# Kernel tuning notes

Hardware: AMD Instinct MI355X
Metric: run time of the kernel (lower is better)

## Reference

```python
import jax, jax.numpy as jnp
import numpy as np

N = 20000      # nodes (all graphs in batch)
E = 320000     # edges (avg degree 16)
G = 16         # graphs in batch
D_IN = 32      # raw node feature dim
D_LAP = 16     # laplacian PE dim
D = 256        # d_model
H = 8          # heads
DH = D // H    # head dim
L = 2          # encoder layers
D_FF = 2 * D   # FFN hidden (FFN_layer1: d_model -> 2*d_model)
EPS = 1e-5


def _layer_norm(x, g, b):
    m = jnp.mean(x, axis=-1, keepdims=True)
    v = jnp.var(x, axis=-1, keepdims=True)
    return g * (x - m) * jax.lax.rsqrt(v + EPS) + b


def setup_inputs() -> dict:
    key = jax.random.key(0)
    ks = jax.random.split(key, 32)

    feat = jax.random.normal(ks[0], (N, D_IN), dtype=jnp.float32)
    lap_pos = jax.random.normal(ks[1], (N, D_LAP), dtype=jnp.float32)
    # random +-1 sign flip per PE dim (done with torch.rand in the original forward)
    sign_flip = jnp.where(jax.random.uniform(ks[2], (D_LAP,)) >= 0.5, 1.0, -1.0).astype(jnp.float32)

    src = jax.random.randint(ks[3], (E,), 0, N, dtype=jnp.int32)
    dst = jax.random.randint(ks[4], (E,), 0, N, dtype=jnp.int32)
    graph_ids = jnp.sort(jax.random.randint(ks[5], (N,), 0, G, dtype=jnp.int32))

    def xavier(k, shape):
        fan_in, fan_out = shape[-2], shape[-1]
        lim = np.sqrt(6.0 / (fan_in + fan_out))
        return jax.random.uniform(k, shape, minval=-lim, maxval=lim, dtype=jnp.float32)

    inp = {
        "feat": feat, "lap_pos": lap_pos, "sign_flip": sign_flip,
        "src": src, "dst": dst, "graph_ids": graph_ids,
        # input embeddings
        "Wh": xavier(ks[6], (D_IN, D)), "bh": jnp.zeros((D,), jnp.float32),
        "Wlp": xavier(ks[7], (D_LAP, D)), "blp": jnp.zeros((D,), jnp.float32),
        # per-layer params, stacked on leading layer axis
        "Wq": xavier(ks[8], (L, D, D)), "Wk": xavier(ks[9], (L, D, D)),
        "Wv": xavier(ks[10], (L, D, D)),
        "Wo": xavier(ks[11], (L, D, D)), "bo": jnp.zeros((L, D), jnp.float32),
        "g1": jnp.ones((L, D), jnp.float32), "b1": jnp.zeros((L, D), jnp.float32),
        "W1": xavier(ks[12], (L, D, D_FF)), "c1": jnp.zeros((L, D_FF), jnp.float32),
        "W2": xavier(ks[13], (L, D_FF, D)), "c2": jnp.zeros((L, D), jnp.float32),
        "g2": jnp.ones((L, D), jnp.float32), "b2": jnp.zeros((L, D), jnp.float32),
    }
    return inp


def _forward(feat, lap_pos, sign_flip, src, dst, graph_ids,
             Wh, bh, Wlp, blp, Wq, Wk, Wv, Wo, bo, g1, b1, W1, c1, W2, c2, g2, b2):
    scale = np.sqrt(DH).astype(np.float32)

    h = feat @ Wh + bh                                  # [N, D]
    h = h + (lap_pos * sign_flip[None, :]) @ Wlp + blp  # add PE embedding

    for l in range(L):
        h_in1 = h
        Q = (h @ Wq[l]).reshape(N, H, DH)
        K = (h @ Wk[l]).reshape(N, H, DH)
        V = (h @ Wv[l]).reshape(N, H, DH)

        # per-edge dot-product score, then exp(clamp(score/sqrt(dh), -5, 5))
        score = jnp.sum(K[src] * Q[dst], axis=-1)                       # [E, H]
        s = jnp.exp(jnp.clip(score / scale, -5.0, 5.0))                # [E, H]

        # segment softmax of s over incoming edges per dst node (F.softmax on mailbox)
        m = jax.ops.segment_max(s, dst, num_segments=N)                 # [N, H], -inf if no in-edges
        p = jnp.exp(s - m[dst])                                         # [E, H]
        den = jax.ops.segment_sum(p, dst, num_segments=N)               # [N, H]
        msg = jax.ops.segment_sum(p[:, :, None] * V[src], dst, num_segments=N)  # [N, H, DH]
        attn = msg / jnp.where(den > 0, den, 1.0)[:, :, None]
        attn = attn.reshape(N, D)

        h = _layer_norm(h_in1 + attn @ Wo[l] + bo[l], g1[l], b1[l])
        h_in2 = h
        ff = jax.nn.relu(h @ W1[l] + c1[l]) @ W2[l] + c2[l]
        h = _layer_norm(h_in2 + ff, g2[l], b2[l])

    # mean readout per graph
    counts = jax.ops.segment_sum(jnp.ones((N,), h.dtype), graph_ids, num_segments=G)
    sums = jax.ops.segment_sum(h, graph_ids, num_segments=G)            # [G, D]
    return sums / jnp.where(counts > 0, counts, 1.0)[:, None]


def reference(feat, lap_pos, sign_flip, src, dst, graph_ids,
              Wh, bh, Wlp, blp, Wq, Wk, Wv, Wo, bo, g1, b1, W1, c1, W2, c2, g2, b2):
    return _forward(feat, lap_pos, sign_flip, src, dst, graph_ids,
                    Wh, bh, Wlp, blp, Wq, Wk, Wv, Wo, bo, g1, b1, W1, c1, W2, c2, g2, b2)
```

## Files before the change

kernel.cpp:

```cpp
#include <hip/hip_runtime.h>
#include <hip/hip_bf16.h>

#define NN   20000
#define EE   320000
#define GG   16
#define DD   256
#define HH   8
#define DHH  32
#define LLAYERS 2
#define DFF  512
#define DIN  32
#define DLAP 16
#define RSPLITS 16

typedef __attribute__((ext_vector_type(8))) short bf16x8;
typedef __attribute__((ext_vector_type(8))) unsigned short u16x8;
typedef __attribute__((ext_vector_type(4))) float f32x4;

__device__ __forceinline__ void gld_lds16(const void* g, void* l) {
  __builtin_amdgcn_global_load_lds((const __attribute__((address_space(1))) uint32_t*)g,
                                   (__attribute__((address_space(3))) uint32_t*)l, 16, 0, 0);
}

__device__ __forceinline__ float b2f(unsigned short s) {
  union { unsigned int i; float f; } u;
  u.i = ((unsigned int)s) << 16;
  return u.f;
}

__device__ __forceinline__ unsigned short f2bu(float f) {
  __hip_bfloat16 b = __float2bfloat16(f);
  return *(unsigned short*)&b;
}

__global__ __launch_bounds__(256) void k_embed(
    const float* __restrict__ feat, const float* __restrict__ lap,
    const float* __restrict__ sign, const float* __restrict__ Wh,
    const float* __restrict__ bh, const float* __restrict__ Wlp,
    const float* __restrict__ blp, float* __restrict__ h,
    __hip_bfloat16* __restrict__ hb) {
  int n = blockIdx.x;
  int d = threadIdx.x;
  float acc = bh[d] + blp[d];
  const float* frow = feat + (size_t)n * DIN;
  const float* lrow = lap + (size_t)n * DLAP;
#pragma unroll
  for (int k = 0; k < DIN; ++k) acc += frow[k] * Wh[k * DD + d];
#pragma unroll
  for (int k = 0; k < DLAP; ++k) acc += (lrow[k] * sign[k]) * Wlp[k * DD + d];
  h[(size_t)n * DD + d] = acc;
  hb[(size_t)n * DD + d] = __float2bfloat16(acc);
}

__global__ __launch_bounds__(256) void k_wt_all(
    const float* __restrict__ Wq, const float* __restrict__ Wk,
    const float* __restrict__ Wv, const float* __restrict__ Wo,
    const float* __restrict__ W1, const float* __restrict__ W2,
    __hip_bfloat16* __restrict__ Wqt, __hip_bfloat16* __restrict__ Wkt,
    __hip_bfloat16* __restrict__ Wvt, __hip_bfloat16* __restrict__ Wot,
    __hip_bfloat16* __restrict__ W1t, __hip_bfloat16* __restrict__ W2t) {
  __shared__ float tile[32][33];
  int z = blockIdx.z;
  const float* in;
  __hip_bfloat16* out;
  int K, N, l;
  if (z < 8) {
    int widx = z >> 1;
    l = z & 1;
    K = DD; N = DD;
    in = (widx == 0) ? Wq : (widx == 1) ? Wk : (widx == 2) ? Wv : Wo;
    out = (widx == 0) ? Wqt : (widx == 1) ? Wkt : (widx == 2) ? Wvt : Wot;
  } else if (z < 10) {
    l = z - 8; K = DD; N = DFF; in = W1; out = W1t;
  } else {
    l = z - 10; K = DFF; N = DD; in = W2; out = W2t;
  }
  int bx = blockIdx.x, by = blockIdx.y;
  if (bx * 32 >= N || by * 32 >= K) return;
  const float* inl = in + (size_t)l * K * N;
  __hip_bfloat16* outl = out + (size_t)l * N * K;
  int tx = threadIdx.x & 31, ty = threadIdx.x >> 5;
#pragma unroll
  for (int i = 0; i < 32; i += 8)
    tile[ty + i][tx] = inl[(size_t)(by * 32 + ty + i) * N + bx * 32 + tx];
  __syncthreads();
#pragma unroll
  for (int i = 0; i < 32; i += 8)
    outl[(size_t)(bx * 32 + ty + i) * K + by * 32 + tx] = __float2bfloat16(tile[tx][ty + i]);
}

template <bool BIAS, bool RELU, bool KVPACK>
__global__ __launch_bounds__(256) void gemm_mfma(
    const __hip_bfloat16* __restrict__ A,
    const __hip_bfloat16* __restrict__ Bt0, const __hip_bfloat16* __restrict__ Bt1,
    const __hip_bfloat16* __restrict__ Bt2,
    const float* __restrict__ bias,
    __hip_bfloat16* __restrict__ C0, __hip_bfloat16* __restrict__ C1,
    int M, int K, int ldc0) {
  const __hip_bfloat16* Bt = (blockIdx.z == 0) ? Bt0 : (blockIdx.z == 1) ? Bt1 : Bt2;
  __hip_bfloat16* Cout = (blockIdx.z == 0) ? C0 : C1;
  const int vo = (blockIdx.z == 2) ? 4 : 0;

  __shared__ short lA[2][4][128][8];
  __shared__ short lB[2][4][128][8];

  const int t = threadIdx.x;
  const int lane = t & 63, w = t >> 6;
  const int bm = blockIdx.x * 128, bn = blockIdx.y * 128;
  const int wr = w >> 1, wc = w & 1;
  const int fr = lane & 15, fg = lane >> 4;

  f32x4 acc[4][4] = {};

  auto stage = [&](int buf, int kt) {
    const int k0 = kt * 32;
#pragma unroll
    for (int it = 0; it < 2; ++it) {
      const int cbase = it * 256 + w * 64;
      const int c = cbase + lane;
      const int g = c >> 7, r = c & 127;
      int arow = bm + r;
      if (arow >= M) arow = M - 1;
      gld_lds16(A + (size_t)arow * K + k0 + g * 8,
                (short*)lA + ((size_t)buf * 512 + cbase) * 8);
      gld_lds16(Bt + (size_t)(bn + r) * K + k0 + g * 8,
                (short*)lB + ((size_t)buf * 512 + cbase) * 8);
    }
  };

  const int nt = K >> 5;
  stage(0, 0);
  for (int kt = 0; kt < nt; ++kt) {
    const int buf = kt & 1;
    __syncthreads();
    if (kt + 1 < nt) stage(buf ^ 1, kt + 1);
    bf16x8 af[4], bfr[4];
#pragma unroll
    for (int i = 0; i < 4; ++i)
      af[i] = *(const bf16x8*)&lA[buf][fg][wr * 64 + i * 16 + fr][0];
#pragma unroll
    for (int j = 0; j < 4; ++j)
      bfr[j] = *(const bf16x8*)&lB[buf][fg][wc * 64 + j * 16 + fr][0];
#pragma unroll
    for (int i = 0; i < 4; ++i)
#pragma unroll
      for (int j = 0; j < 4; ++j)
        acc[i][j] = __builtin_amdgcn_mfma_f32_16x16x32_bf16(af[i], bfr[j], acc[i][j], 0, 0, 0);
  }

#pragma unroll
  for (int i = 0; i < 4; ++i) {
    const int row0 = bm + wr * 64 + i * 16 + fg * 4;
#pragma unroll
    for (int j = 0; j < 4; ++j) {
      const int col = bn + wc * 64 + j * 16 + fr;
      float bv = BIAS ? bias[col] : 0.f;
#pragma unroll
      for (int r = 0; r < 4; ++r) {
        const int row = row0 + r;
        if (row >= M) continue;
        float v = acc[i][j][r] + bv;
        if (RELU) v = fmaxf(v, 0.f);
        if (KVPACK && blockIdx.z != 0) {
          Cout[(size_t)row * (2 * DD) + ((col >> 2) << 3) + vo + (col & 3)] =
              __float2bfloat16(v);
        } else {
          Cout[(size_t)row * ldc0 + col] = __float2bfloat16(v);
        }
      }
    }
  }
}

__global__ __launch_bounds__(256) void gemm_ln(
    const __hip_bfloat16* __restrict__ A,
    const __hip_bfloat16* __restrict__ Bt,
    const float* __restrict__ bias,
    float* __restrict__ h,
    __hip_bfloat16* __restrict__ hb,
    const float* __restrict__ g, const float* __restrict__ b,
    int M, int K) {
  __shared__ short lA[2][4][64][8];
  __shared__ short lB[2][4][256][8];
  __shared__ float redS[64];
  __shared__ float redQ[64];

  const int t = threadIdx.x;
  const int lane = t & 63, w = t >> 6;
  const int bm = blockIdx.x * 64;
  const int fr = lane & 15, fg = lane >> 4;

  if (t < 64) { redS[t] = 0.f; redQ[t] = 0.f; }

  f32x4 acc[4][4] = {};

  auto stage = [&](int buf, int kt) {
    const int k0 = kt * 32;
    {
      int arow = bm + lane;
      if (arow >= M) arow = M - 1;
      gld_lds16(A + (size_t)arow * K + k0 + w * 8,
                (short*)lA + ((size_t)buf * 256 + w * 64) * 8);
    }
#pragma unroll
    for (int it = 0; it < 4; ++it) {
      const int cbase = it * 256 + w * 64;
      const int r = w * 64 + lane;
      gld_lds16(Bt + (size_t)r * K + k0 + it * 8,
                (short*)lB + ((size_t)buf * 1024 + cbase) * 8);
    }
  };

  const int nt = K >> 5;
  stage(0, 0);
  for (int kt = 0; kt < nt; ++kt) {
    const int buf = kt & 1;
    __syncthreads();
    if (kt + 1 < nt) stage(buf ^ 1, kt + 1);
    bf16x8 af[4], bfr[4];
#pragma unroll
    for (int i = 0; i < 4; ++i)
      af[i] = *(const bf16x8*)&lA[buf][fg][i * 16 + fr][0];
#pragma unroll
    for (int j = 0; j < 4; ++j)
      bfr[j] = *(const bf16x8*)&lB[buf][fg][w * 64 + j * 16 + fr][0];
#pragma unroll
    for (int i = 0; i < 4; ++i)
#pragma unroll
      for (int j = 0; j < 4; ++j)
        acc[i][j] = __builtin_amdgcn_mfma_f32_16x16x32_bf16(af[i], bfr[j], acc[i][j], 0, 0, 0);
  }

#pragma unroll
  for (int i = 0; i < 4; ++i) {
#pragma unroll
    for (int r = 0; r < 4; ++r) {
      const int lrow = i * 16 + fg * 4 + r;
      const int grow = bm + lrow;
      float s = 0.f, q = 0.f;
#pragma unroll
      for (int j = 0; j < 4; ++j) {
        const int col = w * 64 + j * 16 + fr;
        float x = acc[i][j][r] + bias[col];
        if (grow < M) x += h[(size_t)grow * DD + col];
        acc[i][j][r] = x;
        s += x;
        q += x * x;
      }
#pragma unroll
      for (int o = 1; o < 16; o <<= 1) {
        s += __shfl_xor(s, o);
        q += __shfl_xor(q, o);
      }
      if (fr == 0) {
        atomicAdd(&redS[lrow], s);
        atomicAdd(&redQ[lrow], q);
      }
    }
  }
  __syncthreads();
#pragma unroll
  for (int i = 0; i < 4; ++i) {
#pragma unroll
    for (int r = 0; r < 4; ++r) {
      const int lrow = i * 16 + fg * 4 + r;
      const int grow = bm + lrow;
      if (grow >= M) continue;
      const float mean = redS[lrow] * (1.f / 256.f);
      const float var = redQ[lrow] * (1.f / 256.f) - mean * mean;
      const float rs = rsqrtf(var + 1e-5f);
#pragma unroll
      for (int j = 0; j < 4; ++j) {
        const int col = w * 64 + j * 16 + fr;
        float v = g[col] * ((acc[i][j][r] - mean) * rs) + b[col];
        h[(size_t)grow * DD + col] = v;
        hb[(size_t)grow * DD + col] = __float2bfloat16(v);
      }
    }
  }
}

__global__ void k_hist(const int* __restrict__ dst, int* __restrict__ deg, int n) {
  int i = blockIdx.x * blockDim.x + threadIdx.x;
  if (i < n) atomicAdd(&deg[dst[i]], 1);
}

__global__ __launch_bounds__(256) void k_scan_block(
    const int* __restrict__ in, int* __restrict__ ex, int* __restrict__ bsum, int n) {
  __shared__ int sm[256];
  int t = threadIdx.x;
  int i = blockIdx.x * 256 + t;
  int v = (i < n) ? in[i] : 0;
  sm[t] = v;
  __syncthreads();
  for (int o = 1; o < 256; o <<= 1) {
    int x = (t >= o) ? sm[t - o] : 0;
    __syncthreads();
    sm[t] += x;
    __syncthreads();
  }
  if (i < n) ex[i] = sm[t] - v;
  if (t == 255) bsum[blockIdx.x] = sm[255];
}

__global__ __launch_bounds__(256) void k_scan_top(
    const int* __restrict__ bsum, int* __restrict__ boff, int nb) {
  __shared__ int sm[256];
  int t = threadIdx.x;
  int v = (t < nb) ? bsum[t] : 0;
  sm[t] = v;
  __syncthreads();
  for (int o = 1; o < 256; o <<= 1) {
    int x = (t >= o) ? sm[t - o] : 0;
    __syncthreads();
    sm[t] += x;
    __syncthreads();
  }
  if (t < nb) boff[t] = sm[t] - v;
}

__global__ void k_finish_indptr(const int* __restrict__ ex, const int* __restrict__ boff,
                                int* __restrict__ indptr, int* __restrict__ cursor,
                                int n, int total) {
  int i = blockIdx.x * 256 + threadIdx.x;
  if (i < n) {
    int v = ex[i] + boff[i >> 8];
    indptr[i] = v;
    cursor[i] = v;
  }
  if (i == 0) indptr[n] = total;
}

__global__ void k_fill(const int* __restrict__ dst, const int* __restrict__ src,
                       int* __restrict__ cursor, int* __restrict__ csr_src, int n) {
  int i = blockIdx.x * blockDim.x + threadIdx.x;
  if (i < n) {
    int pos = atomicAdd(&cursor[dst[i]], 1);
    csr_src[pos] = src[i];
  }
}

__global__ void k_bounds(const int* __restrict__ gid, int* __restrict__ gb, int n) {
  int i = blockIdx.x * blockDim.x + threadIdx.x;
  if (i >= n) return;
  int g = gid[i];
  if (i == 0) {
    for (int x = 0; x <= g; ++x) gb[x] = 0;
  } else {
    int pg = gid[i - 1];
    for (int x = pg + 1; x <= g; ++x) gb[x] = i;
  }
  if (i == n - 1) {
    for (int x = g + 1; x <= GG; ++x) gb[x] = n;
  }
}

__global__ __launch_bounds__(256) void k_attn(
    const int* __restrict__ indptr, const int* __restrict__ csr_src,
    const __hip_bfloat16* __restrict__ Q, const __hip_bfloat16* __restrict__ kvb,
    __hip_bfloat16* __restrict__ attn) {
  int n = blockIdx.x * 4 + (threadIdx.x >> 6);
  if (n >= NN) return;
  int lane = threadIdx.x & 63;
  int half = lane >> 5;
  int sl = lane & 31;
  int doff = sl * 8;
  int s0 = indptr[n], s1 = indptr[n + 1];

  u16x8 qv = *(const u16x8*)((const unsigned short*)Q + (size_t)n * DD + doff);
  float q[8];
#pragma unroll
  for (int i = 0; i < 8; ++i) q[i] = b2f((unsigned short)qv[i]);

  const unsigned short* kvp = (const unsigned short*)kvb;

  float m = 0.f, den = 0.f;
  float a[8] = {};
  int j = s0 + half;
  if (j < s1) {
    const unsigned short* row = kvp + (size_t)csr_src[j] * (2 * DD) + sl * 16;
    u16x8 c0 = *(const u16x8*)row;
    u16x8 c1 = *(const u16x8*)(row + 8);
    for (; j < s1; j += 2) {
      int jn = (j + 2 < s1) ? j + 2 : j;
      const unsigned short* rown = kvp + (size_t)csr_src[jn] * (2 * DD) + sl * 16;
      u16x8 n0 = *(const u16x8*)rown;
      u16x8 n1 = *(const u16x8*)(rown + 8);

      float dot = q[0] * b2f((unsigned short)c0[0]) + q[1] * b2f((unsigned short)c0[1]) +
                  q[2] * b2f((unsigned short)c0[2]) + q[3] * b2f((unsigned short)c0[3]) +
                  q[4] * b2f((unsigned short)c1[0]) + q[5] * b2f((unsigned short)c1[1]) +
                  q[6] * b2f((unsigned short)c1[2]) + q[7] * b2f((unsigned short)c1[3]);
      dot += __shfl_xor(dot, 1);
      dot += __shfl_xor(dot, 2);
      float x = fminf(fmaxf(dot * 0.17677669529663687f, -5.f), 5.f);
      float s = __expf(x);
      if (s - m > 8.f) {
        float r = __expf(m - s);
        den *= r;
#pragma unroll
        for (int i = 0; i < 8; ++i) a[i] *= r;
        m = s;
      }
      float p = __expf(s - m);
      den += p;
      a[0] += p * b2f((unsigned short)c0[4]);
      a[1] += p * b2f((unsigned short)c0[5]);
      a[2] += p * b2f((unsigned short)c0[6]);
      a[3] += p * b2f((unsigned short)c0[7]);
      a[4] += p * b2f((unsigned short)c1[4]);
      a[5] += p * b2f((unsigned short)c1[5]);
      a[6] += p * b2f((unsigned short)c1[6]);
      a[7] += p * b2f((unsigned short)c1[7]);
      c0 = n0;
      c1 = n1;
    }
  }

  float mo = __shfl_xor(m, 32);
  float M = fmaxf(m, mo);
  float r = __expf(m - M);
  den *= r;
#pragma unroll
  for (int i = 0; i < 8; ++i) a[i] *= r;
  den += __shfl_xor(den, 32);
#pragma unroll
  for (int i = 0; i < 8; ++i) a[i] += __shfl_xor(a[i], 32);

  if (half == 0) {
    float inv = 1.f / (den > 0.f ? den : 1.f);
    u16x8 o;
#pragma unroll
    for (int i = 0; i < 8; ++i) o[i] = f2bu(a[i] * inv);
    *(u16x8*)((unsigned short*)attn + (size_t)n * DD + doff) = o;
  }
}

__global__ __launch_bounds__(256) void k_gmean(
    const float* __restrict__ h, const int* __restrict__ gb,
    float* __restrict__ gsum) {
  int g = blockIdx.x, s = blockIdx.y;
  int t = threadIdx.x;
  int r0 = gb[g], r1 = gb[g + 1];
  int len = r1 - r0;
  int per = (len + RSPLITS - 1) / RSPLITS;
  int a = r0 + s * per;
  int b = min(r1, a + per);
  if (a >= b) return;
  float acc = 0.f;
  for (int r = a; r < b; ++r) acc += h[(size_t)r * DD + t];
  atomicAdd(&gsum[g * DD + t], acc);
}

__global__ void k_final(const float* __restrict__ gsum, const int* __restrict__ gb,
                        float* __restrict__ out) {
  int g = blockIdx.x, t = threadIdx.x;
  int len = gb[g + 1] - gb[g];
  out[g * DD + t] = gsum[g * DD + t] / (len > 0 ? (float)len : 1.f);
}

extern "C" void kernel_launch(void* const* d_in, const int* in_sizes, int n_in,
                              void* d_out, int out_size, void* d_ws, size_t ws_size,
                              hipStream_t stream) {
  const float* feat = (const float*)d_in[0];
  const float* lap  = (const float*)d_in[1];
  const float* sign = (const float*)d_in[2];
  const int* srcs   = (const int*)d_in[3];
  const int* dsts   = (const int*)d_in[4];
  const int* gids   = (const int*)d_in[5];
  const float* Wh   = (const float*)d_in[6];
  const float* bh   = (const float*)d_in[7];
  const float* Wlp  = (const float*)d_in[8];
  const float* blp  = (const float*)d_in[9];
  const float* Wq   = (const float*)d_in[10];
  const float* Wk   = (const float*)d_in[11];
  const float* Wv   = (const float*)d_in[12];
  const float* Wo   = (const float*)d_in[13];
  const float* bo   = (const float*)d_in[14];
  const float* g1   = (const float*)d_in[15];
  const float* b1   = (const float*)d_in[16];
  const float* W1   = (const float*)d_in[17];
  const float* c1   = (const float*)d_in[18];
  const float* W2   = (const float*)d_in[19];
  const float* c2   = (const float*)d_in[20];
  const float* g2   = (const float*)d_in[21];
  const float* b2   = (const float*)d_in[22];

  char* base = (char*)d_ws;
  size_t off = 0;
  auto take = [&](size_t bytes) -> void* {
    void* p = base + off;
    off += (bytes + 255) & ~(size_t)255;
    return p;
  };
  float* h      = (float*)take((size_t)NN * DD * 4);
  __hip_bfloat16* hb  = (__hip_bfloat16*)take((size_t)NN * DD * 2);
  __hip_bfloat16* Qb  = (__hip_bfloat16*)take((size_t)NN * DD * 2);
  __hip_bfloat16* kvb = (__hip_bfloat16*)take((size_t)NN * 2 * DD * 2);
  __hip_bfloat16* t1b = (__hip_bfloat16*)take((size_t)NN * DFF * 2);
  __hip_bfloat16* Wqt = (__hip_bfloat16*)take((size_t)LLAYERS * DD * DD * 2);
  __hip_bfloat16* Wkt = (__hip_bfloat16*)take((size_t)LLAYERS * DD * DD * 2);
  __hip_bfloat16* Wvt = (__hip_bfloat16*)take((size_t)LLAYERS * DD * DD * 2);
  __hip_bfloat16* Wot = (__hip_bfloat16*)take((size_t)LLAYERS * DD * DD * 2);
  __hip_bfloat16* W1t = (__hip_bfloat16*)take((size_t)LLAYERS * DD * DFF * 2);
  __hip_bfloat16* W2t = (__hip_bfloat16*)take((size_t)LLAYERS * DFF * DD * 2);
  int* deg     = (int*)take((size_t)NN * 4);
  int* ex      = (int*)take((size_t)NN * 4);
  int* bsum    = (int*)take(256 * 4);
  int* boff    = (int*)take(256 * 4);
  int* indptr  = (int*)take((size_t)(NN + 1) * 4);
  int* cursor  = (int*)take((size_t)NN * 4);
  int* csr_src = (int*)take((size_t)EE * 4);
  int* gb      = (int*)take((size_t)(GG + 1) * 4);
  float* gsum  = (float*)take((size_t)GG * DD * 4);
  __hip_bfloat16* attnb = Qb;

  const int NB = (NN + 255) / 256;

  k_wt_all<<<dim3(DFF / 32, DFF / 32, 12), 256, 0, stream>>>(
      Wq, Wk, Wv, Wo, W1, W2, Wqt, Wkt, Wvt, Wot, W1t, W2t);

  hipMemsetAsync(deg, 0, (size_t)NN * 4, stream);
  k_hist<<<(EE + 255) / 256, 256, 0, stream>>>(dsts, deg, EE);
  k_scan_block<<<NB, 256, 0, stream>>>(deg, ex, bsum, NN);
  k_scan_top<<<1, 256, 0, stream>>>(bsum, boff, NB);
  k_finish_indptr<<<NB, 256, 0, stream>>>(ex, boff, indptr, cursor, NN, EE);
  k_fill<<<(EE + 255) / 256, 256, 0, stream>>>(dsts, srcs, cursor, csr_src, EE);
  k_bounds<<<NB, 256, 0, stream>>>(gids, gb, NN);

  k_embed<<<NN, 256, 0, stream>>>(feat, lap, sign, Wh, bh, Wlp, blp, h, hb);

  const int MB = (NN + 127) / 128;
  const int MB64 = (NN + 63) / 64;
  dim3 gQKV(MB, DD / 128, 3);
  dim3 gF(MB, DFF / 128, 1);

  for (int l = 0; l < LLAYERS; ++l) {
    const __hip_bfloat16* Wqt_l = Wqt + (size_t)l * DD * DD;
    const __hip_bfloat16* Wkt_l = Wkt + (size_t)l * DD * DD;
    const __hip_bfloat16* Wvt_l = Wvt + (size_t)l * DD * DD;
    const __hip_bfloat16* Wot_l = Wot + (size_t)l * DD * DD;
    const __hip_bfloat16* W1t_l = W1t + (size_t)l * DD * DFF;
    const __hip_bfloat16* W2t_l = W2t + (size_t)l * DFF * DD;
    const float* bo_l = bo + (size_t)l * DD;
    const float* g1_l = g1 + (size_t)l * DD;
    const float* b1_l = b1 + (size_t)l * DD;
    const float* c1_l = c1 + (size_t)l * DFF;
    const float* c2_l = c2 + (size_t)l * DD;
    const float* g2_l = g2 + (size_t)l * DD;
    const float* b2_l = b2 + (size_t)l * DD;

    gemm_mfma<false, false, true><<<gQKV, 256, 0, stream>>>(
        hb, Wqt_l, Wkt_l, Wvt_l, nullptr, Qb, kvb, NN, DD, DD);

    k_attn<<<(NN + 3) / 4, 256, 0, stream>>>(indptr, csr_src, Qb, kvb, attnb);

    gemm_ln<<<MB64, 256, 0, stream>>>(attnb, Wot_l, bo_l, h, hb, g1_l, b1_l, NN, DD);

    gemm_mfma<true, true, false><<<gF, 256, 0, stream>>>(
        hb, W1t_l, W1t_l, W1t_l, c1_l, t1b, t1b, NN, DD, DFF);

    gemm_ln<<<MB64, 256, 0, stream>>>(t1b, W2t_l, c2_l, h, hb, g2_l, b2_l, NN, DFF);
  }

  hipMemsetAsync(gsum, 0, (size_t)GG * DD * 4, stream);
  k_gmean<<<dim3(GG, RSPLITS), 256, 0, stream>>>(h, gb, gsum);
  k_final<<<GG, 256, 0, stream>>>(gsum, gb, (float*)d_out);
}
```

Baseline: 496.5 us.

## Replace LDS-staged GEMM+LayerNorm with direct-register loads and 32-row tiles

The fused GEMM+LayerNorm kernel drops its double-buffered LDS staging and per-iteration barriers, and each wave now loads its A and B fragments straight from global memory into registers. The row tile shrinks from 64 to 32, doubling the block count, and K becomes a template parameter so the loop can be unrolled. Bounds checks on M are removed, which relies on NN being a multiple of 32. In exchange, B fragments are no longer shared through LDS across waves, so redundant global and cache traffic goes up.

```diff
diff --git a/kernel.cpp b/kernel.cpp
--- a/kernel.cpp
+++ b/kernel.cpp
@@ -172,6 +172,7 @@
   }
 }
 
+template <int KK>
 __global__ __launch_bounds__(256) void gemm_ln(
     const __hip_bfloat16* __restrict__ A,
     const __hip_bfloat16* __restrict__ Bt,
@@ -179,60 +180,41 @@
     float* __restrict__ h,
     __hip_bfloat16* __restrict__ hb,
     const float* __restrict__ g, const float* __restrict__ b,
-    int M, int K) {
-  __shared__ short lA[2][4][64][8];
-  __shared__ short lB[2][4][256][8];
-  __shared__ float redS[64];
-  __shared__ float redQ[64];
+    int M) {
+  __shared__ float redS[32];
+  __shared__ float redQ[32];
 
   const int t = threadIdx.x;
   const int lane = t & 63, w = t >> 6;
-  const int bm = blockIdx.x * 64;
+  const int bm = blockIdx.x * 32;
   const int fr = lane & 15, fg = lane >> 4;
 
-  if (t < 64) { redS[t] = 0.f; redQ[t] = 0.f; }
-
-  f32x4 acc[4][4] = {};
-
-  auto stage = [&](int buf, int kt) {
+  if (t < 32) { redS[t] = 0.f; redQ[t] = 0.f; }
+
+  f32x4 acc[2][4] = {};
+  const __hip_bfloat16* a0p = A + (size_t)(bm + fr) * KK + fg * 8;
+  const __hip_bfloat16* a1p = A + (size_t)(bm + 16 + fr) * KK + fg * 8;
+  const __hip_bfloat16* bp  = Bt + (size_t)(w * 64 + fr) * KK + fg * 8;
+
+#pragma unroll 2
+  for (int kt = 0; kt < KK / 32; ++kt) {
     const int k0 = kt * 32;
-    {
-      int arow = bm + lane;
-      if (arow >= M) arow = M - 1;
-      gld_lds16(A + (size_t)arow * K + k0 + w * 8,
-                (short*)lA + ((size_t)buf * 256 + w * 64) * 8);
+    bf16x8 af0 = *(const bf16x8*)(a0p + k0);
+    bf16x8 af1 = *(const bf16x8*)(a1p + k0);
+    bf16x8 bfr[4];
+#pragma unroll
+    for (int j = 0; j < 4; ++j)
+      bfr[j] = *(const bf16x8*)(bp + (size_t)j * 16 * KK + k0);
+#pragma unroll
+    for (int j = 0; j < 4; ++j) {
+      acc[0][j] = __builtin_amdgcn_mfma_f32_16x16x32_bf16(af0, bfr[j], acc[0][j], 0, 0, 0);
+      acc[1][j] = __builtin_amdgcn_mfma_f32_16x16x32_bf16(af1, bfr[j], acc[1][j], 0, 0, 0);
     }
-#pragma unroll
-    for (int it = 0; it < 4; ++it) {
-      const int cbase = it * 256 + w * 64;
-      const int r = w * 64 + lane;
-      gld_lds16(Bt + (size_t)r * K + k0 + it * 8,
-                (short*)lB + ((size_t)buf * 1024 + cbase) * 8);
-    }
-  };
-
-  const int nt = K >> 5;
-  stage(0, 0);
-  for (int kt = 0; kt < nt; ++kt) {
-    const int buf = kt & 1;
-    __syncthreads();
-    if (kt + 1 < nt) stage(buf ^ 1, kt + 1);
-    bf16x8 af[4], bfr[4];
-#pragma unroll
-    for (int i = 0; i < 4; ++i)
-      af[i] = *(const bf16x8*)&lA[buf][fg][i * 16 + fr][0];
-#pragma unroll
-    for (int j = 0; j < 4; ++j)
-      bfr[j] = *(const bf16x8*)&lB[buf][fg][w * 64 + j * 16 + fr][0];
-#pragma unroll
-    for (int i = 0; i < 4; ++i)
-#pragma unroll
-      for (int j = 0; j < 4; ++j)
-        acc[i][j] = __builtin_amdgcn_mfma_f32_16x16x32_bf16(af[i], bfr[j], acc[i][j], 0, 0, 0);
-  }
-
-#pragma unroll
-  for (int i = 0; i < 4; ++i) {
+  }
+
+  __syncthreads();
+#pragma unroll
+  for (int i = 0; i < 2; ++i) {
 #pragma unroll
     for (int r = 0; r < 4; ++r) {
       const int lrow = i * 16 + fg * 4 + r;
@@ -241,8 +223,7 @@
 #pragma unroll
       for (int j = 0; j < 4; ++j) {
         const int col = w * 64 + j * 16 + fr;
-        float x = acc[i][j][r] + bias[col];
-        if (grow < M) x += h[(size_t)grow * DD + col];
+        float x = acc[i][j][r] + bias[col] + h[(size_t)grow * DD + col];
         acc[i][j][r] = x;
         s += x;
         q += x * x;
@@ -260,12 +241,11 @@
   }
   __syncthreads();
 #pragma unroll
-  for (int i = 0; i < 4; ++i) {
+  for (int i = 0; i < 2; ++i) {
 #pragma unroll
     for (int r = 0; r < 4; ++r) {
       const int lrow = i * 16 + fg * 4 + r;
       const int grow = bm + lrow;
-      if (grow >= M) continue;
       const float mean = redS[lrow] * (1.f / 256.f);
       const float var = redQ[lrow] * (1.f / 256.f) - mean * mean;
       const float rs = rsqrtf(var + 1e-5f);
@@ -531,7 +511,7 @@
   k_embed<<<NN, 256, 0, stream>>>(feat, lap, sign, Wh, bh, Wlp, blp, h, hb);
 
   const int MB = (NN + 127) / 128;
-  const int MB64 = (NN + 63) / 64;
+  const int MB32 = (NN + 31) / 32;
   dim3 gQKV(MB, DD / 128, 3);
   dim3 gF(MB, DFF / 128, 1);
 
@@ -555,12 +535,12 @@
 
     k_attn<<<(NN + 3) / 4, 256, 0, stream>>>(indptr, csr_src, Qb, kvb, attnb);
 
-    gemm_ln<<<MB64, 256, 0, stream>>>(attnb, Wot_l, bo_l, h, hb, g1_l, b1_l, NN, DD);
+    gemm_ln<DD><<<MB32, 256, 0, stream>>>(attnb, Wot_l, bo_l, h, hb, g1_l, b1_l, NN);
 
     gemm_mfma<true, true, false><<<gF, 256, 0, stream>>>(
         hb, W1t_l, W1t_l, W1t_l, c1_l, t1b, t1b, NN, DD, DFF);
 
-    gemm_ln<<<MB64, 256, 0, stream>>>(t1b, W2t_l, c2_l, h, hb, g2_l, b2_l, NN, DFF);
+    gemm_ln<DFF><<<MB32, 256, 0, stream>>>(t1b, W2t_l, c2_l, h, hb, g2_l, b2_l, NN);
   }
 
   hipMemsetAsync(gsum, 0, (size_t)GG * DD * 4, stream);
```

Result: faster. 457.6 us (-7.8%).
